# Kernel optimization log

Hardware: AMD Instinct MI355X
Metric: run time of the kernel (lower is better)

Reference implementation:

```python
import jax, jax.numpy as jnp
import numpy as np

ORDER = 4          # signature truncation depth
SCALAR_TERM = True # leading 1 term, as in signatory.signature(..., scalar_term=True)
BATCH, STREAM, CHAN = 2048, 128, 5  # channel = path_dim + 1 (time + 4-dim path)


def _exp_levels(dx, m):
    """Tensor exponential of a single increment dx: levels dx^{(x)k}/k!, k=1..m.
    dx: (B, d). Returns list of (B, d**k) arrays."""
    levels = [dx]
    for k in range(2, m + 1):
        prev = levels[-1]  # (B, d**(k-1))
        levels.append((prev[:, :, None] * dx[:, None, :]).reshape(dx.shape[0], -1) / k)
    return levels


def _chen(S, E):
    """Chen's identity: (S tensor-multiply E) truncated to depth m.
    S, E: tuples/lists of (B, d**k) level arrays (level k at list index k-1)."""
    m = len(E)
    B = E[0].shape[0]
    out = []
    for k in range(m):  # output level k+1
        term = S[k] + E[k]
        for i in range(k):  # S level (i+1) tensor E level (k-i)
            a, b = S[i], E[k - 1 - i]
            term = term + (a[:, :, None] * b[:, None, :]).reshape(B, -1)
        out.append(term)
    return tuple(out)


def _signature(path, m, scalar_term):
    """Truncated path signature, flattened levels 1..m (optionally with leading 1).
    path: (B, T, d) -> (B, [1+] d + d^2 + ... + d^m)."""
    B, T, d = path.shape
    dx = jnp.moveaxis(path[:, 1:] - path[:, :-1], 1, 0)  # (T-1, B, d)
    init = tuple(jnp.zeros((B, d ** k), path.dtype) for k in range(1, m + 1))

    def step(S, inc):
        return _chen(S, _exp_levels(inc, m)), None

    S, _ = jax.lax.scan(step, init, dx)
    sig = jnp.concatenate(S, axis=1)
    if scalar_term:
        sig = jnp.concatenate([jnp.ones((B, 1), path.dtype), sig], axis=1)
    return sig


def setup_inputs() -> dict:
    key = jax.random.key(0)
    kx, ky = jax.random.split(key)
    x = jax.random.normal(kx, (BATCH, STREAM, CHAN), dtype=jnp.float32)
    y = jax.random.normal(ky, (BATCH, STREAM, CHAN), dtype=jnp.float32)
    sigma = jnp.ones((CHAN - 1,), dtype=jnp.float32)  # adversarial scaling params
    return {"x": x, "y": y, "sigma": sigma}


def reference(x, y, sigma):
    # adversarial scaling applied to x's non-time channels only (as in forward())
    mu = jnp.concatenate([x[..., :1], x[..., 1:] * sigma], axis=-1)
    nu = y
    # signatures computed once each and shared across kxx, kxy, kyy (same math)
    sx = _signature(mu, ORDER, SCALAR_TERM)  # (B, P)
    sy = _signature(nu, ORDER, SCALAR_TERM)  # (B, P)
    kxx = jnp.einsum('ip,jp->ij', sx, sx)
    kxy = jnp.einsum('ip,jp->ij', sx, sy)
    kyy = jnp.einsum('ip,jp->ij', sy, sy)
    return jnp.mean(kxx) - 2.0 * jnp.mean(kxy) + jnp.mean(kyy)
```

## Files before the change

kernel.cpp:

```cpp
#include <hip/hip_runtime.h>

#define BATCH  2048
#define TLEN   128
#define CH     5
#define NSTEP  127
#define NROW   128
#define SIGDIM 780
#define KACC   16
#define PPB    8
#define NBLK   ((2 * BATCH) / PPB)

__global__ __launch_bounds__(256, 2) void sig_kernel(
    const float* __restrict__ x, const float* __restrict__ y,
    const float* __restrict__ sigma, float* __restrict__ acc,
    unsigned int* __restrict__ counter, float* __restrict__ out) {
  const int tid  = threadIdx.x;
  const int wave = tid >> 6;
  const int lane = tid & 63;
  const int h    = lane >> 5;
  const int u    = lane & 31;
  const bool isX = (blockIdx.x < NBLK / 2);
  const int pbase = (isX ? blockIdx.x : blockIdx.x - NBLK / 2) * PPB;
  const int path  = pbase + wave * 2 + h;
  const float* src = (isX ? x : y) + (size_t)path * (TLEN * CH);

  __shared__ __align__(16) float dxs[PPB][NROW * 8];
  __shared__ float blockAcc[SIGDIM];
  __shared__ float red[4];
  __shared__ unsigned int lastFlag;

  for (int i = tid; i < SIGDIM; i += 256) blockAcc[i] = 0.f;

  float* row = dxs[wave * 2 + h];
  if (u < 8) row[NSTEP * 8 + u] = 0.f;
  for (int i = u; i < NSTEP * CH; i += 32) {
    int t = i / CH, c = i - CH * t;
    float v = src[i + CH] - src[i];
    if (isX && c > 0) v *= sigma[c - 1];
    row[t * 8 + c] = v;
  }
  __syncthreads();

  const int  uc = u < 25 ? u : 24;
  const int  a_ = uc / 5, b_ = uc - 5 * a_;
  const bool act = (u < 25);

  float s1a = 0.f, s2 = 0.f;
  float s3[5] = {0,0,0,0,0};
  float s4[5][5] = {{0,0,0,0,0},{0,0,0,0,0},{0,0,0,0,0},{0,0,0,0,0},{0,0,0,0,0}};

  const float* pa_ = row + a_;
  const float* pb_ = row + b_;

  for (int g = 0; g < 16; ++g) {
    const float* rg = row + g * 64;
    const float* ra = pa_ + g * 64;
    const float* rb = pb_ + g * 64;
    #pragma unroll
    for (int k = 0; k < 8; ++k) {
      const float4 m = *(const float4*)(rg + k * 8);
      const float d0 = m.x, d1 = m.y, d2 = m.z, d3 = m.w;
      const float d4 = rg[k * 8 + 4];
      const float da = ra[k * 8];
      const float db = rb[k * 8];
      const float pa = s1a * (1.f / 6.f) + da * (1.f / 24.f);
      const float qa = s1a * 0.5f        + da * (1.f / 6.f);
      const float ra_ = s1a              + da * 0.5f;
      s1a += da;
      const float p2 = 0.5f * s2 + db * pa;
      const float q2 =        s2 + db * qa;
      s2 += db * ra_;
      #pragma unroll
      for (int c = 0; c < 5; ++c) {
        const float dc = c == 0 ? d0 : c == 1 ? d1 : c == 2 ? d2 : c == 3 ? d3 : d4;
        const float p3 = s3[c] + dc * p2;
        s3[c] += dc * q2;
        s4[c][0] += d0 * p3; s4[c][1] += d1 * p3; s4[c][2] += d2 * p3;
        s4[c][3] += d3 * p3; s4[c][4] += d4 * p3;
      }
    }
  }

  if (act) {
    if (b_ == 0) atomicAdd(&blockAcc[a_], s1a);
    atomicAdd(&blockAcc[5 + uc], s2);
    #pragma unroll
    for (int c = 0; c < 5; ++c) {
      atomicAdd(&blockAcc[30 + uc * 5 + c], s3[c]);
      #pragma unroll
      for (int d = 0; d < 5; ++d)
        atomicAdd(&blockAcc[155 + (uc * 5 + c) * 5 + d], s4[c][d]);
    }
  }
  __syncthreads();

  const float w = isX ? 1.0f : -1.0f;
  float* ap = acc + (size_t)(blockIdx.x & (KACC - 1)) * SIGDIM;
  for (int i = tid; i < SIGDIM; i += 256)
    atomicAdd(ap + i, w * blockAcc[i]);

  __syncthreads();
  if (tid == 0) {
    __threadfence();
    unsigned int old = __hip_atomic_fetch_add(counter, 1u, __ATOMIC_ACQ_REL,
                                              __HIP_MEMORY_SCOPE_AGENT);
    lastFlag = (old == NBLK - 1) ? 1u : 0u;
  }
  __syncthreads();
  if (lastFlag) {
    float local = 0.f;
    for (int i = tid; i < SIGDIM; i += 256) {
      float v = 0.f;
      #pragma unroll
      for (int k = 0; k < KACC; ++k)
        v += __hip_atomic_load(&acc[(size_t)k * SIGDIM + i],
                               __ATOMIC_RELAXED, __HIP_MEMORY_SCOPE_AGENT);
      local += v * v;
    }
    #pragma unroll
    for (int off = 32; off > 0; off >>= 1) local += __shfl_down(local, off, 64);
    if ((tid & 63) == 0) red[tid >> 6] = local;
    __syncthreads();
    if (tid == 0)
      out[0] = (red[0] + red[1] + red[2] + red[3]) / (2048.0f * 2048.0f);
  }
}

extern "C" void kernel_launch(void* const* d_in, const int* in_sizes, int n_in,
                              void* d_out, int out_size, void* d_ws, size_t ws_size,
                              hipStream_t stream) {
  const float* x     = (const float*)d_in[0];
  const float* y     = (const float*)d_in[1];
  const float* sigma = (const float*)d_in[2];
  float* out = (float*)d_out;
  float* acc = (float*)d_ws;
  unsigned int* counter = (unsigned int*)((char*)d_ws + (size_t)KACC * SIGDIM * sizeof(float));

  hipMemsetAsync(d_ws, 0, (size_t)KACC * SIGDIM * sizeof(float) + 64, stream);
  sig_kernel<<<dim3(NBLK), dim3(256), 0, stream>>>(x, y, sigma, acc, counter, out);
}
```

Measured before the change: 113.0 us.

## Split each path into two time segments and combine via Chen identity

```diff
diff --git a/kernel.cpp b/kernel.cpp
--- a/kernel.cpp
+++ b/kernel.cpp
@@ -3,14 +3,13 @@
 #define BATCH  2048
 #define TLEN   128
 #define CH     5
-#define NSTEP  127
-#define NROW   128
 #define SIGDIM 780
 #define KACC   16
-#define PPB    8
+#define PPB    4
 #define NBLK   ((2 * BATCH) / PPB)
+#define SEGR   64
 
-__global__ __launch_bounds__(256, 2) void sig_kernel(
+__global__ __launch_bounds__(256, 4) void sig_kernel(
     const float* __restrict__ x, const float* __restrict__ y,
     const float* __restrict__ sigma, float* __restrict__ acc,
     unsigned int* __restrict__ counter, float* __restrict__ out) {
@@ -21,23 +20,24 @@
   const int u    = lane & 31;
   const bool isX = (blockIdx.x < NBLK / 2);
   const int pbase = (isX ? blockIdx.x : blockIdx.x - NBLK / 2) * PPB;
-  const int path  = pbase + wave * 2 + h;
-  const float* src = (isX ? x : y) + (size_t)path * (TLEN * CH);
+  const int path  = pbase + wave;
+  const float* src = (isX ? x : y) + (size_t)path * (TLEN * CH) + h * (SEGR * CH);
 
-  __shared__ __align__(16) float dxs[PPB][NROW * 8];
+  __shared__ __align__(16) float buf[2 * PPB][784];
   __shared__ float blockAcc[SIGDIM];
   __shared__ float red[4];
   __shared__ unsigned int lastFlag;
 
   for (int i = tid; i < SIGDIM; i += 256) blockAcc[i] = 0.f;
 
-  float* row = dxs[wave * 2 + h];
-  if (u < 8) row[NSTEP * 8 + u] = 0.f;
-  for (int i = u; i < NSTEP * CH; i += 32) {
+  float* bw = buf[wave * 2 + h];
+  if (h == 1 && u < 8) bw[63 * 8 + u] = 0.f;
+  const int lim = h ? 63 * CH : 64 * CH;
+  for (int i = u; i < lim; i += 32) {
     int t = i / CH, c = i - CH * t;
     float v = src[i + CH] - src[i];
     if (isX && c > 0) v *= sigma[c - 1];
-    row[t * 8 + c] = v;
+    bw[t * 8 + c] = v;
   }
   __syncthreads();
 
@@ -49,11 +49,11 @@
   float s3[5] = {0,0,0,0,0};
   float s4[5][5] = {{0,0,0,0,0},{0,0,0,0,0},{0,0,0,0,0},{0,0,0,0,0},{0,0,0,0,0}};
 
-  const float* pa_ = row + a_;
-  const float* pb_ = row + b_;
+  const float* pa_ = bw + a_;
+  const float* pb_ = bw + b_;
 
-  for (int g = 0; g < 16; ++g) {
-    const float* rg = row + g * 64;
+  for (int g = 0; g < 8; ++g) {
+    const float* rg = bw + g * 64;
     const float* ra = pa_ + g * 64;
     const float* rb = pb_ + g * 64;
     #pragma unroll
@@ -65,11 +65,11 @@
       const float db = rb[k * 8];
       const float pa = s1a * (1.f / 6.f) + da * (1.f / 24.f);
       const float qa = s1a * 0.5f        + da * (1.f / 6.f);
-      const float ra_ = s1a              + da * 0.5f;
+      const float rr = s1a               + da * 0.5f;
       s1a += da;
       const float p2 = 0.5f * s2 + db * pa;
       const float q2 =        s2 + db * qa;
-      s2 += db * ra_;
+      s2 += db * rr;
       #pragma unroll
       for (int c = 0; c < 5; ++c) {
         const float dc = c == 0 ? d0 : c == 1 ? d1 : c == 2 ? d2 : c == 3 ? d3 : d4;
@@ -81,15 +81,36 @@
     }
   }
 
-  if (act) {
-    if (b_ == 0) atomicAdd(&blockAcc[a_], s1a);
-    atomicAdd(&blockAcc[5 + uc], s2);
+  if (h == 1 && act) {
+    float* sg = bw;
+    if (b_ == 0) sg[a_] = s1a;
+    sg[5 + uc] = s2;
     #pragma unroll
     for (int c = 0; c < 5; ++c) {
-      atomicAdd(&blockAcc[30 + uc * 5 + c], s3[c]);
+      sg[30 + uc * 5 + c] = s3[c];
       #pragma unroll
-      for (int d = 0; d < 5; ++d)
-        atomicAdd(&blockAcc[155 + (uc * 5 + c) * 5 + d], s4[c][d]);
+      for (int d = 0; d < 5; ++d) sg[155 + (uc * 5 + c) * 5 + d] = s4[c][d];
+    }
+  }
+  __syncthreads();
+
+  if (h == 0 && act) {
+    const float* R = buf[wave * 2 + 1];
+    const float o1 = s1a + R[a_];
+    const float o2 = s2 + s1a * R[b_] + R[5 + uc];
+    if (b_ == 0) atomicAdd(&blockAcc[a_], o1);
+    atomicAdd(&blockAcc[5 + uc], o2);
+    #pragma unroll
+    for (int c = 0; c < 5; ++c) {
+      const float o3 = s3[c] + s2 * R[c] + s1a * R[5 + b_ * 5 + c] + R[30 + uc * 5 + c];
+      atomicAdd(&blockAcc[30 + uc * 5 + c], o3);
+      #pragma unroll
+      for (int d = 0; d < 5; ++d) {
+        const float o4 = s4[c][d] + s3[c] * R[d] + s2 * R[5 + c * 5 + d]
+                       + s1a * R[30 + (b_ * 5 + c) * 5 + d]
+                       + R[155 + (uc * 5 + c) * 5 + d];
+        atomicAdd(&blockAcc[155 + (uc * 5 + c) * 5 + d], o4);
+      }
     }
   }
   __syncthreads();
```

Result: no change. 110.8 us (-1.9%).
